# Kernel tuning notes

Measured on AMD Instinct MI355X. Metric: run time of the kernel, lower is better.

Reference implementation:

```python
import math
import jax, jax.numpy as jnp
import numpy as np

B = 8          # number of graphs in the batch
NMAX = 256     # max nodes per graph (padding size)
K = 128        # num_kernels
H = 32         # num_heads
NTYPE = 101    # max_node_type + 1


def setup_inputs() -> dict:
    key = jax.random.key(0)
    ks = jax.random.split(key, 10)
    sizes = np.asarray(NMAX - np.arange(B) * 16, dtype=np.int32)  # 256,240,...,144 -> ragged
    N = int(sizes.sum())  # 1600
    coord = jax.random.normal(ks[0], (N, 3), dtype=jnp.float32) * 3.0
    node_type = jax.random.randint(ks[1], (N,), 0, NTYPE, dtype=jnp.int32)
    gaussian_means = jax.random.uniform(ks[2], (1, K), minval=0.0, maxval=3.0, dtype=jnp.float32)
    gaussian_stds = jax.random.uniform(ks[3], (1, K), minval=0.0, maxval=3.0, dtype=jnp.float32)
    # nn.Embedding(max_node_type+1, 2) tables; original init is const(0)/const(1),
    # we perturb so the computation is non-degenerate.
    mul_w = jax.random.normal(ks[4], (NTYPE, 2), dtype=jnp.float32) * 0.1
    bias_w = 1.0 + jax.random.normal(ks[5], (NTYPE, 2), dtype=jnp.float32) * 0.1
    W1 = jax.random.normal(ks[6], (K, K), dtype=jnp.float32) / math.sqrt(K)
    b1 = jnp.zeros((K,), dtype=jnp.float32)
    W2 = jax.random.normal(ks[7], (K, H), dtype=jnp.float32) / math.sqrt(K)
    b2 = jnp.zeros((H,), dtype=jnp.float32)
    return {
        "coord": coord,
        "gaussian_means": gaussian_means,
        "gaussian_stds": gaussian_stds,
        "mul_w": mul_w,
        "bias_w": bias_w,
        "W1": W1,
        "b1": b1,
        "W2": W2,
        "b2": b2,
        "node_type": node_type,
        "batch_num_nodes": jnp.asarray(sizes),
    }


def reference(coord, gaussian_means, gaussian_stds, mul_w, bias_w, W1, b1, W2, b2,
              node_type, batch_num_nodes):
    N = coord.shape[0]
    offsets = jnp.concatenate([jnp.zeros((1,), dtype=batch_num_nodes.dtype),
                               jnp.cumsum(batch_num_nodes)[:-1]])
    ar = jnp.arange(NMAX)
    idx = offsets[:, None] + ar[None, :]                     # [B, n] flat node index per graph slot
    valid = ar[None, :] < batch_num_nodes[:, None]           # [B, n] node mask
    idx_c = jnp.clip(idx, 0, N - 1)
    pc = coord[idx_c]                                        # [B, n, 3] padded coords
    pt = node_type[idx_c]                                    # [B, n]

    # pairwise Euclidean distance (torch.cdist p=2), sqrt-safe at 0
    diff = pc[:, :, None, :] - pc[:, None, :, :]             # [B, n, n, 3]
    sq = jnp.sum(diff * diff, axis=-1)                       # [B, n, n]
    nz = sq > 0
    dist = jnp.where(nz, jnp.sqrt(jnp.where(nz, sq, 1.0)), 0.0)

    # outer-sum of per-node (src, dst) scaling embeddings
    mul_e = mul_w[pt]                                        # [B, n, 2]
    bias_e = bias_w[pt]
    mul = mul_e[:, :, None, 0] + mul_e[:, None, :, 1]        # [B, n, n]
    bias = bias_e[:, :, None, 0] + bias_e[:, None, :, 1]
    scaled = mul * dist + bias                               # [B, n, n]

    means = gaussian_means.reshape(-1)                       # [K]
    stds = jnp.abs(gaussian_stds.reshape(-1)) + 0.01         # [K]
    z = (scaled[..., None] - means) / stds                   # [B, n, n, K]
    gk = jnp.exp(-0.5 * z * z) / (-math.sqrt(2.0 * math.pi) * stds)

    h = jax.nn.gelu(gk @ W1 + b1, approximate=False)         # exact gelu like torch F.gelu
    out = h @ W2 + b2                                        # [B, n, n, H]

    pair = valid[:, :, None] & valid[:, None, :]             # padded positions -> -inf
    return jnp.where(pair[..., None], out, -jnp.inf)
```

## Files before the change

kernel.cpp:

```cpp
#include <hip/hip_runtime.h>
#include <math.h>

#define NMAXC 256
#define KC 128
#define HC 32
#define BC 8
#define TP 128
#define NEG_SENTINEL (-1.0e30f)
#define LOG2E 1.4426950408889634f

typedef __bf16 bf16x8 __attribute__((ext_vector_type(8)));
typedef float  f32x16 __attribute__((ext_vector_type(16)));
union FragU { uint4 u; bf16x8 v; };

#if __has_builtin(__builtin_amdgcn_exp2f)
#define EXP2F(x) __builtin_amdgcn_exp2f(x)
#else
#define EXP2F(x) exp2f(x)
#endif

__device__ __forceinline__ unsigned pack2(float lo, float hi) {
    return __builtin_amdgcn_perm(__float_as_uint(hi), __float_as_uint(lo), 0x07060302u);
}

__global__ __launch_bounds__(256) void se3d_prep(const float* __restrict__ W1,
                                                 const float* __restrict__ W2,
                                                 const float* __restrict__ gm,
                                                 const float* __restrict__ gs,
                                                 unsigned* __restrict__ wsu) {
    int t = blockIdx.x * 256 + threadIdx.x;
    if (t < 2048) {
        int fb = t >> 6, lane = t & 63;
        int nt = fb >> 3, ks = fb & 7;
        int n  = nt * 32 + (lane & 31);
        int k0 = ks * 16 + 8 * (lane >> 5);
        unsigned u[4];
#pragma unroll
        for (int p = 0; p < 4; ++p)
            u[p] = pack2(W1[(k0 + 2 * p) * KC + n], W1[(k0 + 2 * p + 1) * KC + n]);
        ((uint4*)wsu)[t] = make_uint4(u[0], u[1], u[2], u[3]);
    } else if (t < 2560) {
        int c = t - 2048;
        int ks = c >> 6, lane = c & 63;
        int n  = lane & 31;
        int k0 = ks * 16 + 8 * (lane >> 5);
        unsigned u[4];
#pragma unroll
        for (int p = 0; p < 4; ++p)
            u[p] = pack2(W2[(k0 + 2 * p) * HC + n], W2[(k0 + 2 * p + 1) * HC + n]);
        ((uint4*)wsu)[2048 + c] = make_uint4(u[0], u[1], u[2], u[3]);
    } else if (t < 2688) {
        int k = t - 2560;
        float inv = 1.0f / (fabsf(gs[k]) + 0.01f);
        float m  = gm[k];
        float A2 = -0.5f * inv * inv * LOG2E;
        float* wf = (float*)wsu + 10240;
        wf[k]       = A2;
        wf[128 + k] = -2.0f * A2 * m;
        wf[256 + k] = A2 * m * m;
        wf[384 + k] = -0.3989422804014327f * inv;
    }
}

__global__ __launch_bounds__(256, 4) void se3d_main(
    const float* __restrict__ coord, const float* __restrict__ mulw,
    const float* __restrict__ biasw, const float* __restrict__ b1,
    const float* __restrict__ b2, const int* __restrict__ ntype,
    const int* __restrict__ bnn, const void* __restrict__ ws,
    float* __restrict__ out)
{
    __shared__ __attribute__((aligned(16))) unsigned short hS[4 * 32 * 136];
    __shared__ float scaled[TP];
    __shared__ int   obase[TP];
    __shared__ float cA[KC], cB[KC], cC[KC], cS[KC];

    const int b = blockIdx.y;
    const int n = bnn[b];
    const int q0 = blockIdx.x * TP;
    const int tid = threadIdx.x;

    if (q0 >= n * n) {
        int v = q0 + (tid >> 1) - n * n;
        int wdt = 256 - n;
        int na = n * wdt;
        int i, j;
        if (v < na) { i = v / wdt; j = n + (v - i * wdt); }
        else        { int vp = v - na; i = n + (vp >> 8); j = vp & 255; }
        float4 s4 = make_float4(NEG_SENTINEL, NEG_SENTINEL, NEG_SENTINEL, NEG_SENTINEL);
        float4* o = (float4*)(out + ((size_t)((b * NMAXC + i) * NMAXC + j)) * HC)
                  + (tid & 1) * 4;
#pragma unroll
        for (int t = 0; t < 4; ++t) o[t] = s4;
        return;
    }

    int off = 0;
    for (int t = 0; t < b; ++t) off += bnn[t];

    const float* wf = (const float*)((const char*)ws + 40960);
    if (tid < KC) {
        cA[tid] = wf[tid];
        cB[tid] = wf[128 + tid];
        cC[tid] = wf[256 + tid];
        cS[tid] = wf[384 + tid];
        int q = q0 + tid;
        int i = q / n;
        int j = q - i * n;
        int gi = off + i, gj = off + j;
        float dx = coord[gi * 3 + 0] - coord[gj * 3 + 0];
        float dy = coord[gi * 3 + 1] - coord[gj * 3 + 1];
        float dz = coord[gi * 3 + 2] - coord[gj * 3 + 2];
        float sq = dx * dx + dy * dy + dz * dz;
        float dist = sq > 0.f ? sqrtf(sq) : 0.f;
        int ti = ntype[gi], tj = ntype[gj];
        scaled[tid] = (mulw[ti * 2 + 0] + mulw[tj * 2 + 1]) * dist
                    + (biasw[ti * 2 + 0] + biasw[tj * 2 + 1]);
        obase[tid]  = ((b * NMAXC + i) * NMAXC + j) * HC;
    }
    __syncthreads();

    const int l = tid & 63, w = tid >> 6;
    const int hi = l >> 5, ln31 = l & 31;
    const int m0 = w * 32;
    const float s = scaled[m0 + ln31];

    const bf16x8* wsW1 = (const bf16x8*)ws;
    const bf16x8* wsW2 = (const bf16x8*)((const char*)ws + 32768);
    const float4* A4 = (const float4*)cA;
    const float4* B4 = (const float4*)cB;
    const float4* C4 = (const float4*)cC;
    const float4* S4 = (const float4*)cS;

    f32x16 acc[4];
#pragma unroll
    for (int nt = 0; nt < 4; ++nt) {
        float b1v = b1[nt * 32 + ln31];
#pragma unroll
        for (int r = 0; r < 16; ++r) acc[nt][r] = b1v;
    }

#pragma unroll
    for (int ks = 0; ks < 8; ++ks) {
        int b4 = ks * 4 + 2 * hi;
        float4 a0 = A4[b4], a1 = A4[b4 + 1];
        float4 q0v = B4[b4], q1 = B4[b4 + 1];
        float4 c0 = C4[b4], c1 = C4[b4 + 1];
        float4 s0 = S4[b4], s1 = S4[b4 + 1];
        float g[8];
        g[0] = s0.x * EXP2F(fmaf(fmaf(a0.x, s, q0v.x), s, c0.x));
        g[1] = s0.y * EXP2F(fmaf(fmaf(a0.y, s, q0v.y), s, c0.y));
        g[2] = s0.z * EXP2F(fmaf(fmaf(a0.z, s, q0v.z), s, c0.z));
        g[3] = s0.w * EXP2F(fmaf(fmaf(a0.w, s, q0v.w), s, c0.w));
        g[4] = s1.x * EXP2F(fmaf(fmaf(a1.x, s, q1.x), s, c1.x));
        g[5] = s1.y * EXP2F(fmaf(fmaf(a1.y, s, q1.y), s, c1.y));
        g[6] = s1.z * EXP2F(fmaf(fmaf(a1.z, s, q1.z), s, c1.z));
        g[7] = s1.w * EXP2F(fmaf(fmaf(a1.w, s, q1.w), s, c1.w));
        FragU a;
        a.u.x = pack2(g[0], g[1]);
        a.u.y = pack2(g[2], g[3]);
        a.u.z = pack2(g[4], g[5]);
        a.u.w = pack2(g[6], g[7]);
#pragma unroll
        for (int nt = 0; nt < 4; ++nt) {
            bf16x8 bb = wsW1[(nt * 8 + ks) * 64 + l];
            acc[nt] = __builtin_amdgcn_mfma_f32_32x32x16_bf16(a.v, bb, acc[nt], 0, 0, 0);
        }
    }

    const float KSG = -1.702f * LOG2E;
    unsigned short* hW = hS + w * (32 * 136);
#pragma unroll
    for (int nt = 0; nt < 4; ++nt) {
#pragma unroll
        for (int r = 0; r < 16; ++r) {
            float x = acc[nt][r];
            float e = EXP2F(x * KSG);
            float gl = x * __builtin_amdgcn_rcpf(1.0f + e);
            int rw = (r & 3) + 8 * (r >> 2) + 4 * hi;
            hW[rw * 136 + nt * 32 + ln31] = (unsigned short)(__float_as_uint(gl) >> 16);
        }
    }

    f32x16 c2;
    {
        float b2v = b2[ln31];
#pragma unroll
        for (int r = 0; r < 16; ++r) c2[r] = b2v;
    }
#pragma unroll
    for (int ks = 0; ks < 8; ++ks) {
        bf16x8 av = *(const bf16x8*)(hW + ln31 * 136 + ks * 16 + 8 * hi);
        bf16x8 bv = wsW2[ks * 64 + l];
        c2 = __builtin_amdgcn_mfma_f32_32x32x16_bf16(av, bv, c2, 0, 0, 0);
    }

#pragma unroll
    for (int r = 0; r < 16; ++r) {
        int m = m0 + (r & 3) + 8 * (r >> 2) + 4 * hi;
        out[(size_t)obase[m] + ln31] = c2[r];
    }
}

extern "C" void kernel_launch(void* const* d_in, const int* in_sizes, int n_in,
                              void* d_out, int out_size, void* d_ws, size_t ws_size,
                              hipStream_t stream) {
    const float* coord = (const float*)d_in[0];
    const float* gm    = (const float*)d_in[1];
    const float* gs    = (const float*)d_in[2];
    const float* mulw  = (const float*)d_in[3];
    const float* biasw = (const float*)d_in[4];
    const float* W1    = (const float*)d_in[5];
    const float* b1    = (const float*)d_in[6];
    const float* W2    = (const float*)d_in[7];
    const float* b2    = (const float*)d_in[8];
    const int* ntype   = (const int*)d_in[9];
    const int* bnn     = (const int*)d_in[10];
    float* out = (float*)d_out;

    hipLaunchKernelGGL(se3d_prep, dim3(11), dim3(256), 0, stream,
                       W1, W2, gm, gs, (unsigned*)d_ws);
    hipLaunchKernelGGL(se3d_main, dim3(NMAXC * NMAXC / TP, BC), dim3(256),
                       0, stream,
                       coord, mulw, biasw, b1, b2, ntype, bnn, d_ws, out);
}
```

Measured before the change: 119.1 us.

## Transpose MFMA operands to keep hidden activations in registers and vectorize stores

The GEMMs are recomputed transposed, with weights as the A operand and the Gaussian features as B. The GELU output then lands in the register layout the second MFMA needs as its B operand, so the shared-memory round trip for the hidden tile goes away. The output accumulator holds heads contiguously per lane, which allows float4 stores instead of scalar scattered stores. The per-kernel scale factor is folded into the exponent (log2 added to the constant term) and W1 is negated, removing one multiply per Gaussian. Pair geometry is now computed per lane instead of through shared memory. The bf16 rounding of the exponent folding changes slightly, and register pressure rises from the 32-element packed hidden array.

```diff
diff --git a/kernel.cpp b/kernel.cpp
--- a/kernel.cpp
+++ b/kernel.cpp
@@ -13,11 +13,7 @@
 typedef float  f32x16 __attribute__((ext_vector_type(16)));
 union FragU { uint4 u; bf16x8 v; };
 
-#if __has_builtin(__builtin_amdgcn_exp2f)
 #define EXP2F(x) __builtin_amdgcn_exp2f(x)
-#else
-#define EXP2F(x) exp2f(x)
-#endif
 
 __device__ __forceinline__ unsigned pack2(float lo, float hi) {
     return __builtin_amdgcn_perm(__float_as_uint(hi), __float_as_uint(lo), 0x07060302u);
@@ -30,35 +26,35 @@
                                                  unsigned* __restrict__ wsu) {
     int t = blockIdx.x * 256 + threadIdx.x;
     if (t < 2048) {
-        int fb = t >> 6, lane = t & 63;
-        int nt = fb >> 3, ks = fb & 7;
-        int n  = nt * 32 + (lane & 31);
-        int k0 = ks * 16 + 8 * (lane >> 5);
+        int f = t >> 6, l = t & 63;
+        int mt = f >> 3, ks = f & 7;
+        int c  = mt * 32 + (l & 31);
+        int k0 = ks * 16 + 8 * (l >> 5);
         unsigned u[4];
 #pragma unroll
         for (int p = 0; p < 4; ++p)
-            u[p] = pack2(W1[(k0 + 2 * p) * KC + n], W1[(k0 + 2 * p + 1) * KC + n]);
+            u[p] = pack2(-W1[(k0 + 2 * p) * KC + c], -W1[(k0 + 2 * p + 1) * KC + c]);
         ((uint4*)wsu)[t] = make_uint4(u[0], u[1], u[2], u[3]);
     } else if (t < 2560) {
-        int c = t - 2048;
-        int ks = c >> 6, lane = c & 63;
-        int n  = lane & 31;
-        int k0 = ks * 16 + 8 * (lane >> 5);
+        int x = t - 2048;
+        int ft = x >> 6, l = x & 63;
+        int hi = l >> 5, ln = l & 31;
         unsigned u[4];
 #pragma unroll
-        for (int p = 0; p < 4; ++p)
-            u[p] = pack2(W2[(k0 + 2 * p) * HC + n], W2[(k0 + 2 * p + 1) * HC + n]);
-        ((uint4*)wsu)[2048 + c] = make_uint4(u[0], u[1], u[2], u[3]);
+        for (int d = 0; d < 4; ++d) {
+            int c0 = 32 * (ft >> 1) + 16 * (ft & 1) + 8 * (d >> 1) + 4 * hi + 2 * (d & 1);
+            u[d] = pack2(W2[c0 * HC + ln], W2[(c0 + 1) * HC + ln]);
+        }
+        ((uint4*)wsu)[2048 + x] = make_uint4(u[0], u[1], u[2], u[3]);
     } else if (t < 2688) {
         int k = t - 2560;
         float inv = 1.0f / (fabsf(gs[k]) + 0.01f);
-        float m  = gm[k];
-        float A2 = -0.5f * inv * inv * LOG2E;
+        float m   = gm[k];
+        float A2  = -0.5f * inv * inv * LOG2E;
         float* wf = (float*)wsu + 10240;
         wf[k]       = A2;
         wf[128 + k] = -2.0f * A2 * m;
-        wf[256 + k] = A2 * m * m;
-        wf[384 + k] = -0.3989422804014327f * inv;
+        wf[256 + k] = A2 * m * m + log2f(0.3989422804014327f * inv);
     }
 }
 
@@ -69,10 +65,7 @@
     const int* __restrict__ bnn, const void* __restrict__ ws,
     float* __restrict__ out)
 {
-    __shared__ __attribute__((aligned(16))) unsigned short hS[4 * 32 * 136];
-    __shared__ float scaled[TP];
-    __shared__ int   obase[TP];
-    __shared__ float cA[KC], cB[KC], cC[KC], cS[KC];
+    __shared__ __attribute__((aligned(16))) float cst[544];
 
     const int b = blockIdx.y;
     const int n = bnn[b];
@@ -94,110 +87,107 @@
         return;
     }
 
+    if (tid < 136) {
+        uint4 v;
+        if (tid < 96)       v = ((const uint4*)((const char*)ws + 40960))[tid];
+        else if (tid < 128) v = ((const uint4*)b1)[tid - 96];
+        else                v = ((const uint4*)b2)[tid - 128];
+        ((uint4*)cst)[tid] = v;
+    }
     int off = 0;
     for (int t = 0; t < b; ++t) off += bnn[t];
-
-    const float* wf = (const float*)((const char*)ws + 40960);
-    if (tid < KC) {
-        cA[tid] = wf[tid];
-        cB[tid] = wf[128 + tid];
-        cC[tid] = wf[256 + tid];
-        cS[tid] = wf[384 + tid];
-        int q = q0 + tid;
-        int i = q / n;
-        int j = q - i * n;
-        int gi = off + i, gj = off + j;
-        float dx = coord[gi * 3 + 0] - coord[gj * 3 + 0];
-        float dy = coord[gi * 3 + 1] - coord[gj * 3 + 1];
-        float dz = coord[gi * 3 + 2] - coord[gj * 3 + 2];
-        float sq = dx * dx + dy * dy + dz * dz;
-        float dist = sq > 0.f ? sqrtf(sq) : 0.f;
-        int ti = ntype[gi], tj = ntype[gj];
-        scaled[tid] = (mulw[ti * 2 + 0] + mulw[tj * 2 + 1]) * dist
-                    + (biasw[ti * 2 + 0] + biasw[tj * 2 + 1]);
-        obase[tid]  = ((b * NMAXC + i) * NMAXC + j) * HC;
-    }
     __syncthreads();
 
     const int l = tid & 63, w = tid >> 6;
-    const int hi = l >> 5, ln31 = l & 31;
-    const int m0 = w * 32;
-    const float s = scaled[m0 + ln31];
-
-    const bf16x8* wsW1 = (const bf16x8*)ws;
-    const bf16x8* wsW2 = (const bf16x8*)((const char*)ws + 32768);
-    const float4* A4 = (const float4*)cA;
-    const float4* B4 = (const float4*)cB;
-    const float4* C4 = (const float4*)cC;
-    const float4* S4 = (const float4*)cS;
+    const int hi = l >> 5, ln = l & 31;
+
+    int q = q0 + w * 32 + ln;
+    int i = q / n;
+    int j = q - i * n;
+    int gi = off + i, gj = off + j;
+    float dx = coord[gi * 3 + 0] - coord[gj * 3 + 0];
+    float dy = coord[gi * 3 + 1] - coord[gj * 3 + 1];
+    float dz = coord[gi * 3 + 2] - coord[gj * 3 + 2];
+    float sq = dx * dx + dy * dy + dz * dz;
+    float dist = sq > 0.f ? sqrtf(sq) : 0.f;
+    int ti = ntype[gi], tj = ntype[gj];
+    float s = (mulw[ti * 2 + 0] + mulw[tj * 2 + 1]) * dist
+            + (biasw[ti * 2 + 0] + biasw[tj * 2 + 1]);
+    size_t obase = ((size_t)((b * NMAXC + i) * NMAXC + j)) * HC;
+
+    const float4*  c4  = (const float4*)cst;
+    const bf16x8*  w1t = (const bf16x8*)ws;
+    const bf16x8*  w2t = (const bf16x8*)((const char*)ws + 32768);
 
     f32x16 acc[4];
 #pragma unroll
-    for (int nt = 0; nt < 4; ++nt) {
-        float b1v = b1[nt * 32 + ln31];
-#pragma unroll
-        for (int r = 0; r < 16; ++r) acc[nt][r] = b1v;
-    }
+    for (int nt = 0; nt < 4; ++nt)
+#pragma unroll
+        for (int qd = 0; qd < 4; ++qd) {
+            float4 bv = c4[96 + 8 * nt + 2 * qd + hi];
+            acc[nt][4 * qd + 0] = bv.x; acc[nt][4 * qd + 1] = bv.y;
+            acc[nt][4 * qd + 2] = bv.z; acc[nt][4 * qd + 3] = bv.w;
+        }
 
 #pragma unroll
     for (int ks = 0; ks < 8; ++ks) {
-        int b4 = ks * 4 + 2 * hi;
-        float4 a0 = A4[b4], a1 = A4[b4 + 1];
-        float4 q0v = B4[b4], q1 = B4[b4 + 1];
-        float4 c0 = C4[b4], c1 = C4[b4 + 1];
-        float4 s0 = S4[b4], s1 = S4[b4 + 1];
+        int b4 = 4 * ks + 2 * hi;
+        float4 a0 = c4[b4],      a1 = c4[b4 + 1];
+        float4 p0 = c4[32 + b4], p1 = c4[32 + b4 + 1];
+        float4 c0 = c4[64 + b4], c1 = c4[64 + b4 + 1];
         float g[8];
-        g[0] = s0.x * EXP2F(fmaf(fmaf(a0.x, s, q0v.x), s, c0.x));
-        g[1] = s0.y * EXP2F(fmaf(fmaf(a0.y, s, q0v.y), s, c0.y));
-        g[2] = s0.z * EXP2F(fmaf(fmaf(a0.z, s, q0v.z), s, c0.z));
-        g[3] = s0.w * EXP2F(fmaf(fmaf(a0.w, s, q0v.w), s, c0.w));
-        g[4] = s1.x * EXP2F(fmaf(fmaf(a1.x, s, q1.x), s, c1.x));
-        g[5] = s1.y * EXP2F(fmaf(fmaf(a1.y, s, q1.y), s, c1.y));
-        g[6] = s1.z * EXP2F(fmaf(fmaf(a1.z, s, q1.z), s, c1.z));
-        g[7] = s1.w * EXP2F(fmaf(fmaf(a1.w, s, q1.w), s, c1.w));
-        FragU a;
-        a.u.x = pack2(g[0], g[1]);
-        a.u.y = pack2(g[2], g[3]);
-        a.u.z = pack2(g[4], g[5]);
-        a.u.w = pack2(g[6], g[7]);
-#pragma unroll
-        for (int nt = 0; nt < 4; ++nt) {
-            bf16x8 bb = wsW1[(nt * 8 + ks) * 64 + l];
-            acc[nt] = __builtin_amdgcn_mfma_f32_32x32x16_bf16(a.v, bb, acc[nt], 0, 0, 0);
+        g[0] = EXP2F(fmaf(fmaf(a0.x, s, p0.x), s, c0.x));
+        g[1] = EXP2F(fmaf(fmaf(a0.y, s, p0.y), s, c0.y));
+        g[2] = EXP2F(fmaf(fmaf(a0.z, s, p0.z), s, c0.z));
+        g[3] = EXP2F(fmaf(fmaf(a0.w, s, p0.w), s, c0.w));
+        g[4] = EXP2F(fmaf(fmaf(a1.x, s, p1.x), s, c1.x));
+        g[5] = EXP2F(fmaf(fmaf(a1.y, s, p1.y), s, c1.y));
+        g[6] = EXP2F(fmaf(fmaf(a1.z, s, p1.z), s, c1.z));
+        g[7] = EXP2F(fmaf(fmaf(a1.w, s, p1.w), s, c1.w));
+        FragU gf;
+        gf.u.x = pack2(g[0], g[1]);
+        gf.u.y = pack2(g[2], g[3]);
+        gf.u.z = pack2(g[4], g[5]);
+        gf.u.w = pack2(g[6], g[7]);
+#pragma unroll
+        for (int mt = 0; mt < 4; ++mt) {
+            bf16x8 af = w1t[(mt * 8 + ks) * 64 + l];
+            acc[mt] = __builtin_amdgcn_mfma_f32_32x32x16_bf16(af, gf.v, acc[mt], 0, 0, 0);
         }
     }
 
     const float KSG = -1.702f * LOG2E;
-    unsigned short* hW = hS + w * (32 * 136);
-#pragma unroll
-    for (int nt = 0; nt < 4; ++nt) {
-#pragma unroll
-        for (int r = 0; r < 16; ++r) {
-            float x = acc[nt][r];
-            float e = EXP2F(x * KSG);
-            float gl = x * __builtin_amdgcn_rcpf(1.0f + e);
-            int rw = (r & 3) + 8 * (r >> 2) + 4 * hi;
-            hW[rw * 136 + nt * 32 + ln31] = (unsigned short)(__float_as_uint(gl) >> 16);
-        }
-    }
+    unsigned hpk[32];
+#pragma unroll
+    for (int nt = 0; nt < 4; ++nt)
+#pragma unroll
+        for (int g8 = 0; g8 < 8; ++g8) {
+            float x0 = acc[nt][2 * g8], x1 = acc[nt][2 * g8 + 1];
+            float gl0 = x0 * __builtin_amdgcn_rcpf(1.0f + EXP2F(x0 * KSG));
+            float gl1 = x1 * __builtin_amdgcn_rcpf(1.0f + EXP2F(x1 * KSG));
+            hpk[nt * 8 + g8] = pack2(gl0, gl1);
+        }
 
     f32x16 c2;
-    {
-        float b2v = b2[ln31];
-#pragma unroll
-        for (int r = 0; r < 16; ++r) c2[r] = b2v;
-    }
-#pragma unroll
-    for (int ks = 0; ks < 8; ++ks) {
-        bf16x8 av = *(const bf16x8*)(hW + ln31 * 136 + ks * 16 + 8 * hi);
-        bf16x8 bv = wsW2[ks * 64 + l];
-        c2 = __builtin_amdgcn_mfma_f32_32x32x16_bf16(av, bv, c2, 0, 0, 0);
-    }
-
-#pragma unroll
-    for (int r = 0; r < 16; ++r) {
-        int m = m0 + (r & 3) + 8 * (r >> 2) + 4 * hi;
-        out[(size_t)obase[m] + ln31] = c2[r];
+#pragma unroll
+    for (int qd = 0; qd < 4; ++qd) {
+        float4 bv = c4[128 + 2 * qd + hi];
+        c2[4 * qd + 0] = bv.x; c2[4 * qd + 1] = bv.y;
+        c2[4 * qd + 2] = bv.z; c2[4 * qd + 3] = bv.w;
+    }
+#pragma unroll
+    for (int t = 0; t < 8; ++t) {
+        FragU hf;
+        int hb = 8 * (t >> 1) + 4 * (t & 1);
+        hf.u = make_uint4(hpk[hb], hpk[hb + 1], hpk[hb + 2], hpk[hb + 3]);
+        bf16x8 a2 = w2t[t * 64 + l];
+        c2 = __builtin_amdgcn_mfma_f32_32x32x16_bf16(a2, hf.v, c2, 0, 0, 0);
+    }
+
+#pragma unroll
+    for (int qd = 0; qd < 4; ++qd) {
+        float4 v = make_float4(c2[4 * qd], c2[4 * qd + 1], c2[4 * qd + 2], c2[4 * qd + 3]);
+        *(float4*)(out + obase + 8 * qd + 4 * hi) = v;
     }
 }
 
```

Measured after the change: 125.3 us. 1.05x slower.
